# Kernel tuning notes

Hardware: AMD Instinct MI355X
Metric: run time of the kernel (lower is better)

Reference implementation:

```python
import jax, jax.numpy as jnp
import numpy as np

DIM_IN = 128; DIM_OUT = 128; DIM_X = 256; L = 256
BATCH = 8192; STD = 0.5; EPS = 1e-3; CRL = 1.0


def setup_inputs() -> dict:
    key = jax.random.key(0)
    ks = jax.random.split(key, 9)
    n = 2 * DIM_X + L
    # trainable params (as in torch __init__)
    X   = jax.random.normal(ks[0], (n, n)) * STD
    Y   = jax.random.normal(ks[1], (DIM_X, DIM_X)) * STD
    B2  = jax.random.normal(ks[2], (DIM_X, DIM_IN)) * STD
    C2  = jax.random.normal(ks[3], (DIM_OUT, DIM_X)) * STD
    D21 = jax.random.normal(ks[4], (DIM_OUT, L)) * STD
    D22 = jax.random.normal(ks[5], (DIM_OUT, DIM_IN)) * STD
    D12 = jax.random.normal(ks[6], (L, DIM_IN)) * STD
    # derived params per update_model_param (stored detached in the torch module)
    H = X.T @ X + EPS * jnp.eye(n)
    H11 = H[:DIM_X, :DIM_X]
    H21 = H[DIM_X:DIM_X + L, :DIM_X]
    H22 = H[DIM_X:DIM_X + L, DIM_X:DIM_X + L]
    H31 = H[DIM_X + L:, :DIM_X]
    H32 = H[DIM_X + L:, DIM_X:DIM_X + L]
    H33 = H[DIM_X + L:, DIM_X + L:]
    Fm  = H31
    B1  = H32
    E   = 0.5 * (H11 + CRL * H33 + Y - Y.T)
    Lam = 0.5 * jnp.diag(H22)            # positive diagonal of Lambda
    D11 = -jnp.tril(H22, -1)             # strictly lower triangular
    C1  = -H21
    x    = jax.random.normal(ks[7], (1, 1, DIM_X)) * 0.1   # internal state (broadcast over batch)
    u_in = jax.random.normal(ks[8], (BATCH, 1, DIM_IN))
    return {"u_in": u_in, "x": x, "Fm": Fm, "B1": B1, "B2": B2, "C1": C1,
            "C2": C2, "D11": D11, "D12": D12, "D21": D21, "D22": D22,
            "E": E, "Lam": Lam}


def ren_forward(u_in, x, Fm, B1, B2, C1, C2, D11, D12, D21, D22, E, Lam):
    batch = u_in.shape[0]
    l = Lam.shape[0]
    # per-step affine terms that do not depend on w (hoisted out of the loop)
    cx = jnp.einsum('li,aoi->l', C1, x)         # (l,)   x has leading dims (1,1)
    du = jnp.einsum('li,boi->lbo', D12, u_in)   # (l,B,1)
    eye = jnp.eye(l, dtype=u_in.dtype)
    w0 = jnp.zeros((batch, 1, l), u_in.dtype)

    # sequential forward substitution: D11 is strictly lower triangular, so
    # step i only reads w columns < i and writes column i.
    def step(w, inp):
        d11_i, lam_i, cx_i, du_i, e_i = inp
        v = cx_i + jnp.einsum('bol,l->bo', w, d11_i) + du_i   # (B,1)
        w = w + e_i * jnp.tanh(v / lam_i)[..., None]          # write column i
        return w, None

    w, _ = jax.lax.scan(step, w0, (D11, Lam, cx, du, eye))    # (B,1,l)

    Einv_T = jnp.linalg.inv(E).T
    x_new = (jnp.einsum('aoi,ji->aoj', x, Fm)
             + jnp.einsum('bol,jl->boj', w, B1)
             + jnp.einsum('boi,ji->boj', u_in, B2)) @ Einv_T  # (B,1,dim_x)
    y = x_new @ C2.T + w @ D21.T + u_in @ D22.T               # (B,1,dim_out)
    return y


def reference(u_in, x, Fm, B1, B2, C1, C2, D11, D12, D21, D22, E, Lam):
    return ren_forward(u_in, x, Fm, B1, B2, C1, C2, D11, D12, D21, D22, E, Lam)
```

## Files before the change

kernel.cpp:

```cpp
#include <hip/hip_runtime.h>
#include <utility>

#define NB 8192

template <typename F, size_t... I>
__device__ __forceinline__ void sfor_impl(F&& f, std::index_sequence<I...>) {
  (f(std::integral_constant<int, (int)I>{}), ...);
}
template <int N, typename F>
__device__ __forceinline__ void sfor(F&& f) {
  sfor_impl((F&&)f, std::make_index_sequence<N>{});
}

constexpr int coff(int li) {
  int o = 0;
  for (int j = 0; j < li; ++j) o += ((63 - j) + 3) & ~3;
  return o;
}
#define CPACK_STRIDE 2176

__device__ __forceinline__ float fast_rcp(float x) {
  float r = __builtin_amdgcn_rcpf(x);
  return r * (2.0f - x * r);
}

__device__ __forceinline__ float fast_tanh(float x) {
  const float e = __expf(2.0f * fminf(x, 40.0f));
  return 1.0f - 2.0f * fast_rcp(e + 1.0f);
}


__device__ void dev_prep(const float* __restrict__ x, const float* __restrict__ C1,
                         const float* __restrict__ Fm, const float* __restrict__ Lam,
                         float* __restrict__ cx, float* __restrict__ xF,
                         float* __restrict__ rLam, int t) {
  float s1 = 0.f, s2 = 0.f;
  for (int i = 0; i < 256; ++i) {
    const float xi = x[i];
    s1 += C1[t * 256 + i] * xi;
    s2 += Fm[t * 256 + i] * xi;
  }
  cx[t] = s1;
  xF[t] = s2;
  rLam[t] = 1.0f / Lam[t];
}

__device__ void dev_pack(const float* __restrict__ D11, float* __restrict__ cpack,
                         int t) {
  const int c = t >> 6;
  const int lane = t & 63;
  int off = 0;
  for (int li = 0; li < 63; ++li) {
    if (lane < 63 - li)
      cpack[c * CPACK_STRIDE + off + lane] =
          D11[(c * 64 + li + 1 + lane) * 256 + (c * 64 + li)];
    off += ((63 - li) + 3) & ~3;
  }
}

__device__ void dev_inv(const float* __restrict__ srcT, int ld,
                        float* __restrict__ dstT, int tid, int s0, int s1) {
  __shared__ float Pcols[128][20];
  __shared__ float MB[128][20];
  __shared__ float Ar[16][132];
  __shared__ float invD[16 * 20];
  const int ti = tid >> 5;
  const int tj = tid & 31;
  const int R = ti * 8, C = tj * 4;
  float a[8][4];
#pragma unroll
  for (int j = 0; j < 4; ++j)
#pragma unroll
    for (int g = 0; g < 2; ++g) {
      const float4 v = *(const float4*)&srcT[(C + j) * ld + (R + 4 * g)];
      a[4 * g + 0][j] = v.x; a[4 * g + 1][j] = v.y;
      a[4 * g + 2][j] = v.z; a[4 * g + 3][j] = v.w;
    }

  for (int s = s0; s < s1; ++s) {
    if ((tj >> 2) == s) {
      const int c0 = C - 16 * s;
#pragma unroll
      for (int i = 0; i < 8; ++i)
        *(float4*)&Pcols[R + i][c0] =
            make_float4(a[i][0], a[i][1], a[i][2], a[i][3]);
    }
    if ((ti >> 1) == s) {
      const int r0 = R - 16 * s;
#pragma unroll
      for (int i = 0; i < 8; ++i)
        *(float4*)&Ar[r0 + i][C] =
            make_float4(a[i][0], a[i][1], a[i][2], a[i][3]);
    }
    __syncthreads();

    if (tid < 16) {
      float q[16];
#pragma unroll
      for (int g = 0; g < 4; ++g) {
        const float4 v = *(const float4*)&Pcols[s * 16 + tid][4 * g];
        q[4 * g] = v.x; q[4 * g + 1] = v.y; q[4 * g + 2] = v.z; q[4 * g + 3] = v.w;
      }
#pragma unroll
      for (int kk = 0; kk < 16; ++kk) {
        float ps[16];
#pragma unroll
        for (int j = 0; j < 16; ++j)
          ps[j] = __int_as_float(
              __builtin_amdgcn_readlane(__float_as_int(q[j]), kk));
        const float piv = fast_rcp(ps[kk]);
#pragma unroll
        for (int j = 0; j < 16; ++j) ps[j] = (j == kk) ? piv : ps[j] * piv;
        const bool isP = (tid == kk);
        const float te = isP ? -1.0f : q[kk];
#pragma unroll
        for (int j = 0; j < 16; ++j) {
          const float base = (isP || j == kk) ? 0.0f : q[j];
          q[j] = base - te * ps[j];
        }
      }
#pragma unroll
      for (int g = 0; g < 4; ++g)
        *(float4*)&invD[tid * 20 + 4 * g] =
            make_float4(q[4 * g], q[4 * g + 1], q[4 * g + 2], q[4 * g + 3]);
    }
    __syncthreads();

    {
      const int r = tid & 127, h = tid >> 7;
      float4 mv;
      if ((r >> 4) == s) {
        mv = *(const float4*)&invD[(r & 15) * 20 + 4 * h];
      } else {
        mv = make_float4(0.f, 0.f, 0.f, 0.f);
#pragma unroll
        for (int g = 0; g < 4; ++g) {
          const float4 p = *(const float4*)&Pcols[r][4 * g];
          const float pc[4] = {p.x, p.y, p.z, p.w};
#pragma unroll
          for (int q = 0; q < 4; ++q) {
            const float4 d = *(const float4*)&invD[(4 * g + q) * 20 + 4 * h];
            mv.x -= pc[q] * d.x; mv.y -= pc[q] * d.y;
            mv.z -= pc[q] * d.z; mv.w -= pc[q] * d.w;
          }
        }
      }
      *(float4*)&MB[r][4 * h] = mv;
    }
    __syncthreads();

    if ((tj >> 2) == s) {
      const int c0 = C - 16 * s;
#pragma unroll
      for (int i = 0; i < 8; ++i) {
        const float4 m = *(const float4*)&MB[R + i][c0];
        a[i][0] = m.x; a[i][1] = m.y; a[i][2] = m.z; a[i][3] = m.w;
      }
    } else {
      if ((ti >> 1) == s) {
#pragma unroll
        for (int i = 0; i < 8; ++i)
#pragma unroll
          for (int j = 0; j < 4; ++j) a[i][j] = 0.f;
      }
#pragma unroll
      for (int half = 0; half < 2; ++half) {
        float4 ar[8];
#pragma unroll
        for (int k = 0; k < 8; ++k)
          ar[k] = *(const float4*)&Ar[half * 8 + k][C];
#pragma unroll
        for (int i = 0; i < 8; ++i) {
          const float4 m0 = *(const float4*)&MB[R + i][half * 8];
          const float4 m1 = *(const float4*)&MB[R + i][half * 8 + 4];
          const float mi[8] = {m0.x, m0.y, m0.z, m0.w, m1.x, m1.y, m1.z, m1.w};
#pragma unroll
          for (int k = 0; k < 8; ++k) {
            a[i][0] += mi[k] * ar[k].x;
            a[i][1] += mi[k] * ar[k].y;
            a[i][2] += mi[k] * ar[k].z;
            a[i][3] += mi[k] * ar[k].w;
          }
        }
      }
    }
    __syncthreads();
  }
#pragma unroll
  for (int j = 0; j < 4; ++j)
#pragma unroll
    for (int g = 0; g < 2; ++g)
      *(float4*)&dstT[(C + j) * 128 + (R + 4 * g)] = make_float4(
          a[4 * g + 0][j], a[4 * g + 1][j], a[4 * g + 2][j], a[4 * g + 3][j]);
}

__device__ void dev_T(const float* __restrict__ u, float* __restrict__ vw, int bid,
                      int t) {
  __shared__ float buf[64 * 65];
  const int b0 = bid * 64;
#pragma unroll
  for (int h = 0; h < 2; ++h) {
#pragma unroll
    for (int q = 0; q < 8; ++q) {
      const int idx = q * 512 + t;
      const int bl = idx >> 6;
      const int i2 = idx & 63;
      buf[i2 * 65 + bl] = u[(b0 + bl) * 128 + 64 * h + i2];
    }
    __syncthreads();
#pragma unroll
    for (int q = 0; q < 8; ++q) {
      const int idx = q * 512 + t;
      const int i2 = idx >> 6;
      const int bl = idx & 63;
      vw[(256 + 64 * h + i2) * NB + b0 + bl] = buf[i2 * 65 + bl];
    }
    __syncthreads();
  }
}

__device__ void dev_du512(const float* __restrict__ D12, const float* __restrict__ cx,
                          float* __restrict__ vw, int bid, int t) {
  __shared__ float Dl[8 * 128];
  const int bx = bid & 3;
  const int l0 = (bid >> 2) * 8;
#pragma unroll
  for (int q = 0; q < 2; ++q) Dl[q * 512 + t] = D12[l0 * 128 + q * 512 + t];
  __syncthreads();
  const float4* vw4 = (const float4*)vw;
  float4* vw4o = (float4*)vw;
  const int b4 = bx * 512 + t;
  float4 acc[8];
#pragma unroll
  for (int j = 0; j < 8; ++j) {
    const float cj = cx[l0 + j];
    acc[j] = make_float4(cj, cj, cj, cj);
  }
#pragma unroll 4
  for (int i = 0; i < 128; ++i) {
    const float4 wv = vw4[(256 + i) * 2048 + b4];
#pragma unroll
    for (int j = 0; j < 8; ++j) {
      const float d = Dl[j * 128 + i];
      acc[j].x += d * wv.x;
      acc[j].y += d * wv.y;
      acc[j].z += d * wv.z;
      acc[j].w += d * wv.w;
    }
  }
#pragma unroll
  for (int j = 0; j < 8; ++j) vw4o[(l0 + j) * 2048 + b4] = acc[j];
}

__device__ void dev_WZ(const float* __restrict__ E, const float* __restrict__ C2,
                       const float* __restrict__ inv1T, float* __restrict__ W,
                       float* __restrict__ z1, int gid) {
  const int half = gid >> 14;
  const int idx = gid & 16383;
  const int j = idx >> 7;
  const int i = idx & 127;
  float s = 0.f;
  if (half == 0) {
    for (int m = 0; m < 128; ++m) s += inv1T[m * 128 + i] * E[(128 + j) * 256 + m];
    W[i * 128 + j] = s;
  } else {
    for (int m = 0; m < 128; ++m) s += inv1T[m * 128 + i] * C2[j * 256 + m];
    z1[i * 128 + j] = s;
  }
}

__device__ void dev_SC(const float* __restrict__ E, const float* __restrict__ C2,
                       const float* __restrict__ W, const float* __restrict__ z1,
                       float* __restrict__ STt, float* __restrict__ c2p, int gid) {
  if (gid < 16384) {
    const int jj = gid >> 7;
    const int i = gid & 127;
    float s = E[(128 + jj) * 256 + 128 + i];
    for (int m = 0; m < 128; ++m) s -= E[m * 256 + 128 + i] * W[m * 128 + jj];
    STt[jj * 128 + i] = s;
  } else {
    const int idx = gid - 16384;
    const int i = idx >> 7;
    const int o = idx & 127;
    float s = C2[o * 256 + 128 + i];
    for (int m = 0; m < 128; ++m) s -= E[m * 256 + 128 + i] * z1[m * 128 + o];
    c2p[i * 128 + o] = s;
  }
}

__device__ void dev_G2(const float* __restrict__ inv2T, const float* __restrict__ c2p,
                       float* __restrict__ g2, int gid) {
  const int i = gid >> 7;
  const int o = gid & 127;
  float s = 0.f;
  for (int m = 0; m < 128; ++m) s += inv2T[m * 128 + i] * c2p[m * 128 + o];
  g2[i * 128 + o] = s;
}

__device__ void dev_G1(const float* __restrict__ W, const float* __restrict__ z1,
                       const float* __restrict__ g2, float* __restrict__ g1, int gid) {
  const int i = gid >> 7;
  const int o = gid & 127;
  float s = z1[i * 128 + o];
  for (int m = 0; m < 128; ++m) s -= W[i * 128 + m] * g2[m * 128 + o];
  g1[i * 128 + o] = s;
}

__device__ void dev_R(const float* __restrict__ B1, const float* __restrict__ B2,
                      const float* __restrict__ D21, const float* __restrict__ D22,
                      const float* __restrict__ g1, const float* __restrict__ g2,
                      const float* __restrict__ xF, float* __restrict__ R,
                      float* __restrict__ y0, int gid) {
  if (gid < 32768) {
    const int o = gid >> 8;
    const int l = gid & 255;
    float s = D21[o * 256 + l];
    for (int m = 0; m < 128; ++m) {
      s += g1[m * 128 + o] * B1[m * 256 + l];
      s += g2[m * 128 + o] * B1[(128 + m) * 256 + l];
    }
    R[o * 384 + l] = s;
  } else if (gid < 49152) {
    const int t2 = gid - 32768;
    const int o = t2 >> 7;
    const int i = t2 & 127;
    float s = D22[o * 128 + i];
    for (int m = 0; m < 128; ++m) {
      s += g1[m * 128 + o] * B2[m * 128 + i];
      s += g2[m * 128 + o] * B2[(128 + m) * 128 + i];
    }
    R[o * 384 + 256 + i] = s;
  } else if (gid < 49280) {
    const int o = gid - 49152;
    float s = 0.f;
    for (int m = 0; m < 128; ++m) {
      s += g1[m * 128 + o] * xF[m];
      s += g2[m * 128 + o] * xF[128 + m];
    }
    y0[o] = s;
  }
}

__device__ void dev_scan(const float* __restrict__ cpack,
                         const float* __restrict__ rLam, float* __restrict__ vw,
                         int c, int bid, int t) {
  __shared__ float sc[CPACK_STRIDE];
  __shared__ float srl[64];
  for (int i = t; i < CPACK_STRIDE; i += 512) sc[i] = cpack[c * CPACK_STRIDE + i];
  if (t < 64) srl[t] = rLam[c * 64 + t];
  __syncthreads();
  if (t >= 256) return;

  const int b = bid * 256 + t;
  const int l0 = c * 64;
  const float4* cp4 = (const float4*)sc;
  float v[64];
#pragma unroll
  for (int li = 0; li < 64; ++li) v[li] = vw[(l0 + li) * NB + b];
  sfor<64>([&](auto LI) {
    constexpr int li = decltype(LI)::value;
    const float w = fast_tanh(v[li] * srl[li]);
    vw[(l0 + li) * NB + b] = w;
    constexpr int n = 63 - li;
    constexpr int off4 = coff(li) / 4;
    sfor<(n + 3) / 4>([&](auto Q) {
      constexpr int q = decltype(Q)::value;
      const float4 d = cp4[off4 + q];
      if constexpr (4 * q + 0 < n) v[li + 1 + 4 * q + 0] += d.x * w;
      if constexpr (4 * q + 1 < n) v[li + 1 + 4 * q + 1] += d.y * w;
      if constexpr (4 * q + 2 < n) v[li + 1 + 4 * q + 2] += d.z * w;
      if constexpr (4 * q + 3 < n) v[li + 1 + 4 * q + 3] += d.w * w;
    });
  });
}

__device__ void dev_upd(const float* __restrict__ D11, float* __restrict__ vw, int c,
                        int role, int lane) {
  float4* vw4 = (float4*)vw;
  const int b4 = (role & 7) * 256 + lane;
  const int lp0 = (c + 1) * 64 + (role >> 3) * 8;
  const int k0 = c * 64;
  float4 acc[8];
#pragma unroll
  for (int j = 0; j < 8; ++j) acc[j] = vw4[(lp0 + j) * 2048 + b4];
  for (int k = 0; k < 64; ++k) {
    const float4 wv = vw4[(k0 + k) * 2048 + b4];
#pragma unroll
    for (int j = 0; j < 8; ++j) {
      const float d = D11[(lp0 + j) * 256 + k0 + k];
      acc[j].x += d * wv.x;
      acc[j].y += d * wv.y;
      acc[j].z += d * wv.z;
      acc[j].w += d * wv.w;
    }
  }
#pragma unroll
  for (int j = 0; j < 8; ++j) vw4[(lp0 + j) * 2048 + b4] = acc[j];
}


__global__ __launch_bounds__(512) void mega1(const float* u, const float* x,
                                             const float* C1, const float* Fm,
                                             const float* Lam, const float* D11,
                                             const float* E, float* vw, float* cx,
                                             float* xF, float* rLam, float* cpack,
                                             float* invSt) {
  const int bid = blockIdx.x;
  const int t = threadIdx.x;
  if (bid < 128) {
    dev_T(u, vw, bid, t);
  } else if (bid == 128) {
    if (t < 256) dev_prep(x, C1, Fm, Lam, cx, xF, rLam, t);
  } else if (bid == 129) {
    if (t < 256) dev_pack(D11, cpack, t);
  } else {
    dev_inv(E, 256, invSt, t, 0, 4);
  }
}

__global__ __launch_bounds__(512) void mega2(const float* D12, const float* cx,
                                             float* vw, const float* invSt,
                                             float* inv1T) {
  const int bid = blockIdx.x;
  const int t = threadIdx.x;
  if (bid < 128) dev_du512(D12, cx, vw, bid, t);
  else dev_inv(invSt, 128, inv1T, t, 4, 8);
}

__global__ __launch_bounds__(512) void mega3(const float* cpack, const float* rLam,
                                             float* vw, const float* E,
                                             const float* C2, const float* inv1T,
                                             float* W, float* z1) {
  const int bid = blockIdx.x;
  const int t = threadIdx.x;
  if (bid < 32) {
    dev_scan(cpack, rLam, vw, 0, bid, t);
  } else {
    dev_WZ(E, C2, inv1T, W, z1, (bid - 32) * 512 + t);
  }
}

__global__ __launch_bounds__(512) void mega4(const float* D11, float* vw,
                                             const float* E, const float* C2,
                                             const float* W, const float* z1,
                                             float* STt, float* c2p) {
  const int bid = blockIdx.x;
  const int t = threadIdx.x;
  if (bid < 96) dev_upd(D11, vw, 0, bid * 2 + (t >> 8), t & 255);
  else dev_SC(E, C2, W, z1, STt, c2p, (bid - 96) * 512 + t);
}

__global__ __launch_bounds__(512) void mega5(const float* cpack, const float* rLam,
                                             float* vw, const float* STt,
                                             float* inv2St) {
  const int bid = blockIdx.x;
  const int t = threadIdx.x;
  if (bid < 32) {
    dev_scan(cpack, rLam, vw, 1, bid, t);
  } else {
    dev_inv(STt, 128, inv2St, t, 0, 4);
  }
}

__global__ __launch_bounds__(512) void mega6(const float* D11, float* vw,
                                             const float* inv2St, float* inv2T) {
  const int bid = blockIdx.x;
  const int t = threadIdx.x;
  if (bid < 64) dev_upd(D11, vw, 1, bid * 2 + (t >> 8), t & 255);
  else dev_inv(inv2St, 128, inv2T, t, 4, 8);
}

__global__ __launch_bounds__(512) void mega7(const float* cpack, const float* rLam,
                                             float* vw, const float* inv2T,
                                             const float* c2p, float* g2) {
  const int bid = blockIdx.x;
  const int t = threadIdx.x;
  if (bid < 32) {
    dev_scan(cpack, rLam, vw, 2, bid, t);
  } else {
    dev_G2(inv2T, c2p, g2, (bid - 32) * 512 + t);
  }
}

__global__ __launch_bounds__(512) void mega8(const float* D11, float* vw,
                                             const float* W, const float* z1,
                                             const float* g2, float* g1) {
  const int bid = blockIdx.x;
  const int t = threadIdx.x;
  if (bid < 32) dev_upd(D11, vw, 2, bid * 2 + (t >> 8), t & 255);
  else dev_G1(W, z1, g2, g1, (bid - 32) * 512 + t);
}

__global__ __launch_bounds__(512) void mega9(const float* cpack, const float* rLam,
                                             float* vw, const float* B1,
                                             const float* B2, const float* D21,
                                             const float* D22, const float* g1,
                                             const float* g2, const float* xF,
                                             float* R, float* y0) {
  const int bid = blockIdx.x;
  const int t = threadIdx.x;
  if (bid < 32) {
    dev_scan(cpack, rLam, vw, 3, bid, t);
  } else {
    dev_R(B1, B2, D21, D22, g1, g2, xF, R, y0, (bid - 32) * 512 + t);
  }
}

__global__ __launch_bounds__(256) void k_y(const float* __restrict__ vw,
                                           const float* __restrict__ R,
                                           const float* __restrict__ y0,
                                           float* __restrict__ y) {
  __shared__ float Rl[768];
  const int tid = threadIdx.x;
  const int bid = blockIdx.x;
  const int gx = bid & 7;
  const int gy = bid >> 3;
  const int o0 = gy * 2;
#pragma unroll
  for (int q = 0; q < 3; ++q) Rl[q * 256 + tid] = R[o0 * 384 + q * 256 + tid];
  __syncthreads();

  const float4* vw4 = (const float4*)vw;
  const int b4 = gx * 256 + tid;
  float acc[4][2];
#pragma unroll
  for (int j = 0; j < 2; ++j) {
    const float y0j = y0[o0 + j];
#pragma unroll
    for (int bi = 0; bi < 4; ++bi) acc[bi][j] = y0j;
  }
  for (int k = 0; k < 384; k += 8) {
    float4 w[8];
#pragma unroll
    for (int kk = 0; kk < 8; ++kk) w[kk] = vw4[(k + kk) * 2048 + b4];
#pragma unroll
    for (int j = 0; j < 2; ++j) {
      const float4 r0 = *(const float4*)&Rl[j * 384 + k];
      const float4 r1 = *(const float4*)&Rl[j * 384 + k + 4];
      acc[0][j] += r0.x * w[0].x + r0.y * w[1].x + r0.z * w[2].x + r0.w * w[3].x +
                   r1.x * w[4].x + r1.y * w[5].x + r1.z * w[6].x + r1.w * w[7].x;
      acc[1][j] += r0.x * w[0].y + r0.y * w[1].y + r0.z * w[2].y + r0.w * w[3].y +
                   r1.x * w[4].y + r1.y * w[5].y + r1.z * w[6].y + r1.w * w[7].y;
      acc[2][j] += r0.x * w[0].z + r0.y * w[1].z + r0.z * w[2].z + r0.w * w[3].z +
                   r1.x * w[4].z + r1.y * w[5].z + r1.z * w[6].z + r1.w * w[7].z;
      acc[3][j] += r0.x * w[0].w + r0.y * w[1].w + r0.z * w[2].w + r0.w * w[3].w +
                   r1.x * w[4].w + r1.y * w[5].w + r1.z * w[6].w + r1.w * w[7].w;
    }
  }
  const int b0 = b4 * 4;
#pragma unroll
  for (int bi = 0; bi < 4; ++bi) {
    *(float2*)&y[(b0 + bi) * 128 + o0] = make_float2(acc[bi][0], acc[bi][1]);
  }
}

extern "C" void kernel_launch(void* const* d_in, const int* in_sizes, int n_in,
                              void* d_out, int out_size, void* d_ws, size_t ws_size,
                              hipStream_t stream) {
  const float* u   = (const float*)d_in[0];
  const float* x   = (const float*)d_in[1];
  const float* Fm  = (const float*)d_in[2];
  const float* B1  = (const float*)d_in[3];
  const float* B2  = (const float*)d_in[4];
  const float* C1  = (const float*)d_in[5];
  const float* C2  = (const float*)d_in[6];
  const float* D11 = (const float*)d_in[7];
  const float* D12 = (const float*)d_in[8];
  const float* D21 = (const float*)d_in[9];
  const float* D22 = (const float*)d_in[10];
  const float* E   = (const float*)d_in[11];
  const float* Lam = (const float*)d_in[12];
  float* y = (float*)d_out;

  float* F = (float*)d_ws;
  float* vw    = F;
  float* SMb   = F + 384 * NB;
  float* inv1T = SMb;
  float* Wm    = SMb + 16384;
  float* z1    = SMb + 32768;
  float* STt   = SMb + 49152;
  float* c2p   = SMb + 65536;
  float* inv2T = SMb + 81920;
  float* g2    = SMb + 98304;
  float* g1    = SMb + 114688;
  float* Rm    = SMb + 131072;
  float* y0v   = SMb + 180224;
  float* cx    = SMb + 180352;
  float* xF    = SMb + 180608;
  float* rLam  = SMb + 180864;
  float* cpack = SMb + 181120;
  float* invSt  = STt;
  float* inv2St = g1;

  mega1<<<131, 512, 0, stream>>>(u, x, C1, Fm, Lam, D11, E, vw, cx, xF, rLam,
                                 cpack, invSt);
  mega2<<<129, 512, 0, stream>>>(D12, cx, vw, invSt, inv1T);
  mega3<<<96, 512, 0, stream>>>(cpack, rLam, vw, E, C2, inv1T, Wm, z1);
  mega4<<<160, 512, 0, stream>>>(D11, vw, E, C2, Wm, z1, STt, c2p);
  mega5<<<33, 512, 0, stream>>>(cpack, rLam, vw, STt, inv2St);
  mega6<<<65, 512, 0, stream>>>(D11, vw, inv2St, inv2T);
  mega7<<<64, 512, 0, stream>>>(cpack, rLam, vw, inv2T, c2p, g2);
  mega8<<<64, 512, 0, stream>>>(D11, vw, Wm, z1, g2, g1);
  mega9<<<129, 512, 0, stream>>>(cpack, rLam, vw, B1, B2, D21, D22, g1, g2, xF,
                                 Rm, y0v);
  k_y<<<512, 256, 0, stream>>>(vw, Rm, y0v, y);
}
```

Baseline: 334.3 us.

## Split-K the final output GEMM with atomic accumulation and zero y early

```diff
diff --git a/kernel.cpp b/kernel.cpp
--- a/kernel.cpp
+++ b/kernel.cpp
@@ -217,6 +217,14 @@
     }
     __syncthreads();
   }
+}
+
+__device__ void dev_yz(float* __restrict__ y, int role, int t) {
+  float4* y4 = (float4*)y;
+  const int idx0 = role * 512 + t;
+  const float4 z = make_float4(0.f, 0.f, 0.f, 0.f);
+#pragma unroll
+  for (int q = 0; q < 16; ++q) y4[q * 16384 + idx0] = z;
 }
 
 __device__ void dev_du512(const float* __restrict__ D12, const float* __restrict__ cx,
@@ -404,7 +412,7 @@
                                              const float* Lam, const float* D11,
                                              const float* E, float* vw, float* cx,
                                              float* xF, float* rLam, float* cpack,
-                                             float* invSt) {
+                                             float* invSt, float* y) {
   const int bid = blockIdx.x;
   const int t = threadIdx.x;
   if (bid < 128) {
@@ -413,8 +421,10 @@
     if (t < 256) dev_prep(x, C1, Fm, Lam, cx, xF, rLam, t);
   } else if (bid == 129) {
     if (t < 256) dev_pack(D11, cpack, t);
+  } else if (bid == 130) {
+    dev_inv(E, 256, invSt, t, 0, 4);
   } else {
-    dev_inv(E, 256, invSt, t, 0, 4);
+    dev_yz(y, bid - 131, t);
   }
 }
 
@@ -514,29 +524,36 @@
   const int tid = threadIdx.x;
   const int bid = blockIdx.x;
   const int gx = bid & 7;
-  const int gy = bid >> 3;
-  const int o0 = gy * 2;
-#pragma unroll
-  for (int q = 0; q < 3; ++q) Rl[q * 256 + tid] = R[o0 * 384 + q * 256 + tid];
+  const int gy = (bid >> 3) & 31;
+  const int ks = bid >> 8;
+  const int o0 = gy * 4;
+  const int kbase = ks * 192;
+#pragma unroll
+  for (int q = 0; q < 3; ++q) {
+    const int e = q * 256 + tid;
+    const int j = e / 192;
+    const int kk = e - j * 192;
+    Rl[e] = R[(o0 + j) * 384 + kbase + kk];
+  }
   __syncthreads();
 
   const float4* vw4 = (const float4*)vw;
   const int b4 = gx * 256 + tid;
-  float acc[4][2];
-#pragma unroll
-  for (int j = 0; j < 2; ++j) {
-    const float y0j = y0[o0 + j];
-#pragma unroll
-    for (int bi = 0; bi < 4; ++bi) acc[bi][j] = y0j;
-  }
-  for (int k = 0; k < 384; k += 8) {
+  float acc[4][4];
+#pragma unroll
+  for (int j = 0; j < 4; ++j) {
+    const float init = (ks == 0) ? y0[o0 + j] : 0.f;
+#pragma unroll
+    for (int bi = 0; bi < 4; ++bi) acc[bi][j] = init;
+  }
+  for (int k = 0; k < 192; k += 8) {
     float4 w[8];
 #pragma unroll
-    for (int kk = 0; kk < 8; ++kk) w[kk] = vw4[(k + kk) * 2048 + b4];
-#pragma unroll
-    for (int j = 0; j < 2; ++j) {
-      const float4 r0 = *(const float4*)&Rl[j * 384 + k];
-      const float4 r1 = *(const float4*)&Rl[j * 384 + k + 4];
+    for (int kk = 0; kk < 8; ++kk) w[kk] = vw4[(kbase + k + kk) * 2048 + b4];
+#pragma unroll
+    for (int j = 0; j < 4; ++j) {
+      const float4 r0 = *(const float4*)&Rl[j * 192 + k];
+      const float4 r1 = *(const float4*)&Rl[j * 192 + k + 4];
       acc[0][j] += r0.x * w[0].x + r0.y * w[1].x + r0.z * w[2].x + r0.w * w[3].x +
                    r1.x * w[4].x + r1.y * w[5].x + r1.z * w[6].x + r1.w * w[7].x;
       acc[1][j] += r0.x * w[0].y + r0.y * w[1].y + r0.z * w[2].y + r0.w * w[3].y +
@@ -549,9 +566,10 @@
   }
   const int b0 = b4 * 4;
 #pragma unroll
-  for (int bi = 0; bi < 4; ++bi) {
-    *(float2*)&y[(b0 + bi) * 128 + o0] = make_float2(acc[bi][0], acc[bi][1]);
-  }
+  for (int bi = 0; bi < 4; ++bi)
+#pragma unroll
+    for (int j = 0; j < 4; ++j)
+      atomicAdd(&y[(b0 + bi) * 128 + o0 + j], acc[bi][j]);
 }
 
 extern "C" void kernel_launch(void* const* d_in, const int* in_sizes, int n_in,
@@ -592,8 +610,8 @@
   float* invSt  = STt;
   float* inv2St = g1;
 
-  mega1<<<131, 512, 0, stream>>>(u, x, C1, Fm, Lam, D11, E, vw, cx, xF, rLam,
-                                 cpack, invSt);
+  mega1<<<163, 512, 0, stream>>>(u, x, C1, Fm, Lam, D11, E, vw, cx, xF, rLam,
+                                 cpack, invSt, y);
   mega2<<<129, 512, 0, stream>>>(D12, cx, vw, invSt, inv1T);
   mega3<<<96, 512, 0, stream>>>(cpack, rLam, vw, E, C2, inv1T, Wm, z1);
   mega4<<<160, 512, 0, stream>>>(D11, vw, E, C2, Wm, z1, STt, c2p);
```

Measured after the change: 414.4 us. 1.24x slower.

## Split k_y reduction across two half-blocks and widen output tile to four columns

Applied to the files above, without the earlier changes.

```diff
diff --git a/kernel.cpp b/kernel.cpp
--- a/kernel.cpp
+++ b/kernel.cpp
@@ -506,37 +506,40 @@
   }
 }
 
-__global__ __launch_bounds__(256) void k_y(const float* __restrict__ vw,
+__global__ __launch_bounds__(512) void k_y(const float* __restrict__ vw,
                                            const float* __restrict__ R,
                                            const float* __restrict__ y0,
                                            float* __restrict__ y) {
-  __shared__ float Rl[768];
+  __shared__ float Rl[1536];
+  __shared__ float part[256 * 16];
   const int tid = threadIdx.x;
   const int bid = blockIdx.x;
   const int gx = bid & 7;
   const int gy = bid >> 3;
-  const int o0 = gy * 2;
-#pragma unroll
-  for (int q = 0; q < 3; ++q) Rl[q * 256 + tid] = R[o0 * 384 + q * 256 + tid];
+  const int o0 = gy * 4;
+#pragma unroll
+  for (int q = 0; q < 3; ++q) Rl[q * 512 + tid] = R[o0 * 384 + q * 512 + tid];
   __syncthreads();
 
+  const int lane = tid & 255;
+  const int ks = tid >> 8;
+  const int kbase = ks * 192;
   const float4* vw4 = (const float4*)vw;
-  const int b4 = gx * 256 + tid;
-  float acc[4][2];
-#pragma unroll
-  for (int j = 0; j < 2; ++j) {
-    const float y0j = y0[o0 + j];
-#pragma unroll
-    for (int bi = 0; bi < 4; ++bi) acc[bi][j] = y0j;
-  }
-  for (int k = 0; k < 384; k += 8) {
+  const int b4 = gx * 256 + lane;
+  float acc[4][4];
+#pragma unroll
+  for (int j = 0; j < 4; ++j)
+#pragma unroll
+    for (int bi = 0; bi < 4; ++bi) acc[bi][j] = 0.f;
+
+  for (int k = 0; k < 192; k += 8) {
     float4 w[8];
 #pragma unroll
-    for (int kk = 0; kk < 8; ++kk) w[kk] = vw4[(k + kk) * 2048 + b4];
-#pragma unroll
-    for (int j = 0; j < 2; ++j) {
-      const float4 r0 = *(const float4*)&Rl[j * 384 + k];
-      const float4 r1 = *(const float4*)&Rl[j * 384 + k + 4];
+    for (int kk = 0; kk < 8; ++kk) w[kk] = vw4[(kbase + k + kk) * 2048 + b4];
+#pragma unroll
+    for (int j = 0; j < 4; ++j) {
+      const float4 r0 = *(const float4*)&Rl[j * 384 + kbase + k];
+      const float4 r1 = *(const float4*)&Rl[j * 384 + kbase + k + 4];
       acc[0][j] += r0.x * w[0].x + r0.y * w[1].x + r0.z * w[2].x + r0.w * w[3].x +
                    r1.x * w[4].x + r1.y * w[5].x + r1.z * w[6].x + r1.w * w[7].x;
       acc[1][j] += r0.x * w[0].y + r0.y * w[1].y + r0.z * w[2].y + r0.w * w[3].y +
@@ -547,10 +550,25 @@
                    r1.x * w[4].w + r1.y * w[5].w + r1.z * w[6].w + r1.w * w[7].w;
     }
   }
-  const int b0 = b4 * 4;
-#pragma unroll
-  for (int bi = 0; bi < 4; ++bi) {
-    *(float2*)&y[(b0 + bi) * 128 + o0] = make_float2(acc[bi][0], acc[bi][1]);
+
+  if (ks == 1) {
+#pragma unroll
+    for (int bi = 0; bi < 4; ++bi)
+      *(float4*)&part[lane * 16 + bi * 4] =
+          make_float4(acc[bi][0], acc[bi][1], acc[bi][2], acc[bi][3]);
+  }
+  __syncthreads();
+  if (ks == 0) {
+    const int b0 = b4 * 4;
+#pragma unroll
+    for (int bi = 0; bi < 4; ++bi) {
+      const float4 p = *(const float4*)&part[lane * 16 + bi * 4];
+      *(float4*)&y[(b0 + bi) * 128 + o0] =
+          make_float4(acc[bi][0] + p.x + y0[o0 + 0],
+                      acc[bi][1] + p.y + y0[o0 + 1],
+                      acc[bi][2] + p.z + y0[o0 + 2],
+                      acc[bi][3] + p.w + y0[o0 + 3]);
+    }
   }
 }
 
@@ -603,5 +621,5 @@
   mega8<<<64, 512, 0, stream>>>(D11, vw, Wm, z1, g2, g1);
   mega9<<<129, 512, 0, stream>>>(cpack, rLam, vw, B1, B2, D21, D22, g1, g2, xF,
                                  Rm, y0v);
-  k_y<<<512, 256, 0, stream>>>(vw, Rm, y0v, y);
-}
+  k_y<<<256, 512, 0, stream>>>(vw, Rm, y0v, y);
+}
```

Measured after the change: 321.0 us. 1.04x faster.
